# Performance work log

Hardware: AMD Instinct MI355X
Metric: run time of the kernel (lower is better)

Reference implementation:

```python
import jax, jax.numpy as jnp
import numpy as np

T = 5          # temporal frames
WS = 8         # window size (square)
HEADS = 6
DIM = 192      # output channels; qkv input channels = 3*DIM
SHIFT = WS // 2
HDIM = DIM // HEADS
SCALE = HDIM ** -0.5
N = T * WS * WS  # tokens per window = 320


def _rel_index():
    # Faithful replication of the torch buffer construction (including the
    # quirk that the dw channel gets no offset).
    coords = np.stack(np.meshgrid(np.arange(T), np.arange(WS), np.arange(WS), indexing='ij'))
    cf = coords.reshape(3, -1)                      # (3, N)
    rel = (cf[:, :, None] - cf[:, None, :]).transpose(1, 2, 0).astype(np.int64)
    rel[:, :, 0] += WS - 1                          # dt channel
    rel[:, :, 1] += WS - 1                          # dh channel
    rel[:, :, 0] *= 2 * WS - 1
    return rel.sum(-1)                               # (N, N) int

REL_INDEX = jnp.asarray(_rel_index())


def setup_inputs() -> dict:
    key = jax.random.key(0)
    k1, k2, k3, k4 = jax.random.split(key, 4)
    B, H, W = 2, 64, 64
    C = 3 * DIM
    qkv = jax.random.normal(k1, (B, T * H * W, C), jnp.float32)
    bias_table = jax.random.normal(k2, ((T * 2 * WS - 1) * (2 * WS - 1), HEADS), jnp.float32) * 0.02
    proj_w = jax.random.normal(k3, (DIM, DIM), jnp.float32) / np.sqrt(DIM)
    proj_b = jax.random.normal(k4, (DIM,), jnp.float32) * 0.01
    # Standard Swin shifted-window attention mask, tiled over T (t-outer order).
    img = np.zeros((H, W), np.float32)
    cnt = 0
    sls = (slice(0, -WS), slice(-WS, -SHIFT), slice(-SHIFT, None))
    for hs in sls:
        for ws_ in sls:
            img[hs, ws_] = cnt
            cnt += 1
    mw = img.reshape(H // WS, WS, W // WS, WS).transpose(0, 2, 1, 3).reshape(-1, WS * WS)
    mw = np.tile(mw, (1, T))                         # (nW, N)
    am = mw[:, None, :] - mw[:, :, None]
    mask = jnp.asarray(np.where(am != 0, -100.0, 0.0).astype(np.float32))
    return {'qkv': qkv, 'bias_table': bias_table, 'proj_w': proj_w,
            'proj_b': proj_b, 'mask': mask, 'H': H, 'W': W}


def reference(qkv, bias_table, proj_w, proj_b, mask, H, W):
    B, L, C = qkv.shape
    x = qkv.reshape(B, T, H, W, C)
    # cyclic shift
    x = jnp.roll(x, shift=(-SHIFT, -SHIFT), axis=(2, 3))
    # window partition -> (B*nW, N, C)
    x = x.reshape(B, T, H // WS, WS, W // WS, WS, C)
    x = x.transpose(0, 2, 4, 1, 3, 5, 6).reshape(-1, N, C)
    B_ = x.shape[0]
    qkv_ = x.reshape(B_, N, 3, HEADS, HDIM).transpose(2, 0, 3, 1, 4)  # (3,B_,h,N,d)
    q, k, v = qkv_[0] * SCALE, qkv_[1], qkv_[2]
    attn = jnp.einsum('bhqd,bhkd->bhqk', q, k)       # (B_, h, N, N)
    rpb = bias_table[REL_INDEX.reshape(-1)].reshape(N, N, HEADS).transpose(2, 0, 1)
    attn = attn + rpb[None]
    nW = mask.shape[0]
    attn = attn.reshape(B_ // nW, nW, HEADS, N, N) + mask[None, :, None]
    attn = jax.nn.softmax(attn.reshape(B_, HEADS, N, N), axis=-1)
    out = jnp.einsum('bhqk,bhkd->bhqd', attn, v)     # (B_, h, N, d)
    out = out.transpose(0, 2, 1, 3).reshape(B_, N, DIM)
    out = out @ proj_w.T + proj_b
    # window reverse -> (B, T, H, W, DIM)
    out = out.reshape(B, H // WS, W // WS, T, WS, WS, DIM)
    out = out.transpose(0, 3, 1, 4, 2, 5, 6).reshape(B, T, H, W, DIM)
    out = jnp.roll(out, shift=(SHIFT, SHIFT), axis=(2, 3))
    return out.reshape(B, T * H * W, DIM)
```

## Files before the change

kernel.cpp:

```cpp
#include <hip/hip_runtime.h>
#include <hip/hip_bf16.h>

#define TT      5
#define NHEADS  6
#define DIMC    192
#define SHIFT_  4
#define HDIM_   32
#define NTOK    320
#define NWIN    64
#define BATCH   2
#define LOG2E   1.44269504088896f
#define SCALE_LOG2E (0.17677669529663687f * 1.44269504088896f)
#define NEGMASK (-100.0f * 1.44269504088896f)

typedef short short8v __attribute__((ext_vector_type(8)));
typedef float floatx4 __attribute__((ext_vector_type(4)));
union FragU { uint4 u; short8v s; };

static __device__ __forceinline__ float bf16lo(unsigned u) {
    union { unsigned i; float f; } x; x.i = u << 16; return x.f;
}
static __device__ __forceinline__ float bf16hi(unsigned u) {
    union { unsigned i; float f; } x; x.i = u & 0xffff0000u; return x.f;
}
static __device__ __forceinline__ unsigned short bf16b(float f) {
    __hip_bfloat16 h = __float2bfloat16(f);
    unsigned short u; __builtin_memcpy(&u, &h, 2); return u;
}
static __device__ __forceinline__ unsigned pk2(float a, float b) {
    return (unsigned)bf16b(a) | ((unsigned)bf16b(b) << 16);
}
static __device__ __forceinline__ unsigned pk2h(float a, float b) {
    unsigned ua = __float_as_uint(a), ub = __float_as_uint(b);
    return ((ua + 0x8000u) >> 16) | ((ub + 0x8000u) & 0xffff0000u);
}
static __device__ __forceinline__ float fexp2(float x) {
    float r;
    asm("v_exp_f32 %0, %1" : "=v"(r) : "v"(x));
    return r;
}

static __device__ __forceinline__ bool detect_bf16(const unsigned* q) {
    uint4 w = ((const uint4*)q)[threadIdx.x & 63];
    int cnt = 0;
    unsigned e;
    e = (w.x >> 7) & 0xffu; cnt += (e >= 100u && e <= 135u);
    e = (w.y >> 7) & 0xffu; cnt += (e >= 100u && e <= 135u);
    e = (w.z >> 7) & 0xffu; cnt += (e >= 100u && e <= 135u);
    e = (w.w >> 7) & 0xffu; cnt += (e >= 100u && e <= 135u);
    unsigned long long m = __ballot(cnt >= 2);
    return __popcll(m) >= 32;
}

__global__ __launch_bounds__(NTOK) void attn_mfma(
    const void* __restrict__ qkv_raw,
    const float* __restrict__ rpb,
    __hip_bfloat16* __restrict__ win_out)
{
    const bool isbf = detect_bf16((const unsigned*)qkv_raw);
    const int bid = blockIdx.x;
    const int b_  = bid / NHEADS;
    const int h   = bid - b_ * NHEADS;
    const int bb  = b_ >> 6;
    const int wdx = b_ & 63;
    const int wi  = wdx >> 3, wj = wdx & 7;
    const int tid = threadIdx.x;
    const int w    = tid >> 6;
    const int lane = tid & 63;
    const int l15  = lane & 15;
    const int quad = lane >> 4;
    const int g    = lane >> 3;
    const int li   = lane & 7;

    __shared__ unsigned short sVT[32 * 328];

    {
        const int btok = w * 64;
        if (!isbf) {
            const float* q32 = (const float*)qkv_raw;
            #pragma unroll
            for (int r = 0; r < 8; r++) {
                const int token = btok + r * 8 + g;
                const int t = token >> 6, s = token & 63;
                const int gh = (wi * 8 + (s >> 3) + SHIFT_) & 63;
                const int gw = (wj * 8 + (s & 7) + SHIFT_) & 63;
                const long grow = (long)bb * (TT * 64 * 64) + t * 4096 + gh * 64 + gw;
                const float4 vv = *(const float4*)(q32 + grow * (3 * DIMC) + 2 * DIMC + h * HDIM_ + li * 4);
                const int d0 = li * 4;
                sVT[(d0 + 0) * 328 + token] = bf16b(vv.x);
                sVT[(d0 + 1) * 328 + token] = bf16b(vv.y);
                sVT[(d0 + 2) * 328 + token] = bf16b(vv.z);
                sVT[(d0 + 3) * 328 + token] = bf16b(vv.w);
            }
        } else {
            const unsigned short* q16 = (const unsigned short*)qkv_raw;
            #pragma unroll
            for (int r = 0; r < 8; r++) {
                const int token = btok + r * 8 + g;
                const int t = token >> 6, s = token & 63;
                const int gh = (wi * 8 + (s >> 3) + SHIFT_) & 63;
                const int gw = (wj * 8 + (s & 7) + SHIFT_) & 63;
                const long grow = (long)bb * (TT * 64 * 64) + t * 4096 + gh * 64 + gw;
                const uint2 vv = *(const uint2*)(q16 + grow * (3 * DIMC) + 2 * DIMC + h * HDIM_ + li * 4);
                const int d0 = li * 4;
                sVT[(d0 + 0) * 328 + token] = (unsigned short)(vv.x & 0xffffu);
                sVT[(d0 + 1) * 328 + token] = (unsigned short)(vv.x >> 16);
                sVT[(d0 + 2) * 328 + token] = (unsigned short)(vv.y & 0xffffu);
                sVT[(d0 + 3) * 328 + token] = (unsigned short)(vv.y >> 16);
            }
        }
    }

    FragU qf[4];
    int labq[4];
    const float* rq[4];
    #pragma unroll
    for (int jq = 0; jq < 4; jq++) {
        const int qtok = w * 64 + jq * 16 + l15;
        const int t = qtok >> 6, s = qtok & 63, hl = s >> 3, wl = s & 7;
        rq[jq] = rpb + ((h * NTOK + qtok) * NTOK);
        const int hh = wi * 8 + hl, ww = wj * 8 + wl;
        labq[jq] = ((hh < 56) ? 0 : ((hh < 60) ? 1 : 2)) * 3 +
                   ((ww < 56) ? 0 : ((ww < 60) ? 1 : 2));
        const int gh = (wi * 8 + hl + SHIFT_) & 63;
        const int gw = (wj * 8 + wl + SHIFT_) & 63;
        const long grow = (long)bb * (TT * 64 * 64) + t * 4096 + gh * 64 + gw;
        if (!isbf) {
            const float* qp = (const float*)qkv_raw + grow * (3 * DIMC) + h * HDIM_ + quad * 8;
            qf[jq].u = make_uint4(
                pk2(qp[0]*SCALE_LOG2E, qp[1]*SCALE_LOG2E), pk2(qp[2]*SCALE_LOG2E, qp[3]*SCALE_LOG2E),
                pk2(qp[4]*SCALE_LOG2E, qp[5]*SCALE_LOG2E), pk2(qp[6]*SCALE_LOG2E, qp[7]*SCALE_LOG2E));
        } else {
            const uint4 uu = *(const uint4*)((const __hip_bfloat16*)qkv_raw + grow * (3 * DIMC) + h * HDIM_ + quad * 8);
            qf[jq].u = make_uint4(
                pk2(bf16lo(uu.x)*SCALE_LOG2E, bf16hi(uu.x)*SCALE_LOG2E),
                pk2(bf16lo(uu.y)*SCALE_LOG2E, bf16hi(uu.y)*SCALE_LOG2E),
                pk2(bf16lo(uu.z)*SCALE_LOG2E, bf16hi(uu.z)*SCALE_LOG2E),
                pk2(bf16lo(uu.w)*SCALE_LOG2E, bf16hi(uu.w)*SCALE_LOG2E));
        }
    }
    __syncthreads();

    const int koff0 = ((l15 >> 2) << 3) + (l15 & 3);

    const floatx4 z4 = {0.f, 0.f, 0.f, 0.f};
    floatx4 oacc[4][2];
    #pragma unroll
    for (int i = 0; i < 4; i++) { oacc[i][0] = z4; oacc[i][1] = z4; }
    float rs[4] = {0.f, 0.f, 0.f, 0.f};

    for (int kb = 0; kb < 10; kb++) {
        FragU kf0, kf1;
        {
            const int tok0 = kb * 32 + koff0;
            const int t0 = tok0 >> 6, s0 = tok0 & 63;
            const int gh0 = (wi * 8 + (s0 >> 3) + SHIFT_) & 63;
            const int gw0 = (wj * 8 + (s0 & 7) + SHIFT_) & 63;
            const long grow0 = (long)bb * (TT * 64 * 64) + t0 * 4096 + gh0 * 64 + gw0;
            const int tok1 = tok0 + 4;
            const int t1 = tok1 >> 6, s1 = tok1 & 63;
            const int gh1 = (wi * 8 + (s1 >> 3) + SHIFT_) & 63;
            const int gw1 = (wj * 8 + (s1 & 7) + SHIFT_) & 63;
            const long grow1 = (long)bb * (TT * 64 * 64) + t1 * 4096 + gh1 * 64 + gw1;
            if (!isbf) {
                const float* kp0 = (const float*)qkv_raw + grow0 * (3 * DIMC) + DIMC + h * HDIM_ + quad * 8;
                const float* kp1 = (const float*)qkv_raw + grow1 * (3 * DIMC) + DIMC + h * HDIM_ + quad * 8;
                const float4 a0 = *(const float4*)kp0, b0 = *(const float4*)(kp0 + 4);
                const float4 a1 = *(const float4*)kp1, b1 = *(const float4*)(kp1 + 4);
                kf0.u = make_uint4(pk2(a0.x, a0.y), pk2(a0.z, a0.w), pk2(b0.x, b0.y), pk2(b0.z, b0.w));
                kf1.u = make_uint4(pk2(a1.x, a1.y), pk2(a1.z, a1.w), pk2(b1.x, b1.y), pk2(b1.z, b1.w));
            } else {
                kf0.u = *(const uint4*)((const __hip_bfloat16*)qkv_raw + grow0 * (3 * DIMC) + DIMC + h * HDIM_ + quad * 8);
                kf1.u = *(const uint4*)((const __hip_bfloat16*)qkv_raw + grow1 * (3 * DIMC) + DIMC + h * HDIM_ + quad * 8);
            }
        }

        FragU vf0, vf1;
        vf0.u = *(const uint4*)&sVT[l15 * 328 + kb * 32 + quad * 8];
        vf1.u = *(const uint4*)&sVT[(16 + l15) * 328 + kb * 32 + quad * 8];

        float4 rb0[4], rb1[4];
        #pragma unroll
        for (int jq = 0; jq < 4; jq++) {
            const float* rp = rq[jq] + kb * 32 + quad * 8;
            rb0[jq] = *(const float4*)rp;
            rb1[jq] = *(const float4*)(rp + 4);
        }

        floatx4 sv0[4], sv1[4];
        #pragma unroll
        for (int jq = 0; jq < 4; jq++)
            sv0[jq] = __builtin_amdgcn_mfma_f32_16x16x32_bf16(kf0.s, qf[jq].s, z4, 0, 0, 0);
        #pragma unroll
        for (int jq = 0; jq < 4; jq++)
            sv1[jq] = __builtin_amdgcn_mfma_f32_16x16x32_bf16(kf1.s, qf[jq].s, z4, 0, 0, 0);

        const int sh   = (kb & 1) * 4 + quad;
        const int rhk  = (wi == 7) ? ((sh < 4) ? 1 : 2) : 0;
        const int lab0 = rhk * 3 + ((wj == 7) ? 1 : 0);
        const int lab1 = rhk * 3 + ((wj == 7) ? 2 : 0);

        #pragma unroll
        for (int jq = 0; jq < 4; jq++) {
            const float m0 = (lab0 != labq[jq]) ? NEGMASK : 0.f;
            const float m1 = (lab1 != labq[jq]) ? NEGMASK : 0.f;
            float e0[4], e1[4];
            e0[0] = fexp2(sv0[jq][0] + rb0[jq].x + m0);
            e0[1] = fexp2(sv0[jq][1] + rb0[jq].y + m0);
            e0[2] = fexp2(sv0[jq][2] + rb0[jq].z + m0);
            e0[3] = fexp2(sv0[jq][3] + rb0[jq].w + m0);
            e1[0] = fexp2(sv1[jq][0] + rb1[jq].x + m1);
            e1[1] = fexp2(sv1[jq][1] + rb1[jq].y + m1);
            e1[2] = fexp2(sv1[jq][2] + rb1[jq].z + m1);
            e1[3] = fexp2(sv1[jq][3] + rb1[jq].w + m1);
            rs[jq] += ((e0[0] + e0[1]) + (e0[2] + e0[3]))
                    + ((e1[0] + e1[1]) + (e1[2] + e1[3]));
            FragU pf;
            pf.u.x = pk2h(e0[0], e0[1]); pf.u.y = pk2h(e0[2], e0[3]);
            pf.u.z = pk2h(e1[0], e1[1]); pf.u.w = pk2h(e1[2], e1[3]);
            oacc[jq][0] = __builtin_amdgcn_mfma_f32_16x16x32_bf16(vf0.s, pf.s, oacc[jq][0], 0, 0, 0);
            oacc[jq][1] = __builtin_amdgcn_mfma_f32_16x16x32_bf16(vf1.s, pf.s, oacc[jq][1], 0, 0, 0);
        }
    }

    unsigned short* wp = (unsigned short*)win_out;
    #pragma unroll
    for (int jq = 0; jq < 4; jq++) {
        float r = rs[jq];
        r += __shfl_xor(r, 16);
        r += __shfl_xor(r, 32);
        const float inv = 1.0f / r;
        const long ob = ((long)b_ * NTOK + (w * 64 + jq * 16 + l15)) * DIMC + h * HDIM_ + quad * 4;
        #pragma unroll
        for (int nt = 0; nt < 2; nt++) {
            const floatx4 o = oacc[jq][nt];
            *(uint2*)&wp[ob + nt * 16] =
                make_uint2(pk2(o[0] * inv, o[1] * inv), pk2(o[2] * inv, o[3] * inv));
        }
    }
}

__global__ __launch_bounds__(256) void prep_all(
    const void* __restrict__ w_raw, const void* __restrict__ b_raw,
    const void* __restrict__ bias_raw,
    const unsigned* __restrict__ sniff,
    unsigned short* __restrict__ wbf, float* __restrict__ bf32,
    float* __restrict__ rpb)
{
    const bool isbf = detect_bf16(sniff);
    const int g = blockIdx.x * 256 + threadIdx.x;
    if (g < 36864) {
        if (!isbf) wbf[g] = bf16b(((const float*)w_raw)[g]);
        else       wbf[g] = ((const unsigned short*)w_raw)[g];
    }
    if (g < 192) {
        bf32[g] = isbf
            ? __bfloat162float(((const __hip_bfloat16*)b_raw)[g])
            : ((const float*)b_raw)[g];
    }
    const int h = g / (NTOK * NTOK);
    const int r = g - h * (NTOK * NTOK);
    const int q = r / NTOK;
    const int k = r - q * NTOK;
    const int cnq = (q >> 6) * 15 + ((q >> 3) & 7) + (q & 7);
    const int cnk = (k >> 6) * 15 + ((k >> 3) & 7) + (k & 7);
    const int idx = (cnq - cnk + 112) * NHEADS + h;
    const float v = isbf
        ? __bfloat162float(((const __hip_bfloat16*)bias_raw)[idx])
        : ((const float*)bias_raw)[idx];
    rpb[g] = v * LOG2E;
}

__global__ __launch_bounds__(256) void proj_mfma(
    const __hip_bfloat16* __restrict__ win,
    const unsigned short* __restrict__ wbf,
    const float* __restrict__ bf32,
    const unsigned* __restrict__ sniff,
    void* __restrict__ out_raw)
{
    const bool isbf = detect_bf16(sniff);
    const int tid  = threadIdx.x;
    const int w    = tid >> 6;
    const int lane = tid & 63;
    const int l15  = lane & 15;
    const int quad = lane >> 4;
    const int tok0 = blockIdx.x * 64 + w * 16;

    __shared__ unsigned short sX[64 * 200];

    {
        const unsigned short* src = (const unsigned short*)win
                                  + (long)blockIdx.x * 64 * DIMC;
        #pragma unroll
        for (int it = 0; it < 6; it++) {
            const int j   = it * 256 + tid;
            const int tok = j / 24;
            const int d8  = j - tok * 24;
            const uint4 v = *(const uint4*)(src + j * 8);
            *(uint4*)&sX[tok * 200 + d8 * 8] = v;
        }
    }
    __syncthreads();

    const floatx4 z4 = {0.f, 0.f, 0.f, 0.f};
    floatx4 acc[12];
    #pragma unroll
    for (int nt = 0; nt < 12; nt++) acc[nt] = z4;

    #pragma unroll
    for (int ks = 0; ks < 6; ks++) {
        FragU xf;
        xf.u = *(const uint4*)&sX[(w * 16 + l15) * 200 + ks * 32 + quad * 8];
        #pragma unroll
        for (int nt = 0; nt < 12; nt++) {
            FragU wf;
            wf.u = *(const uint4*)(wbf + (nt * 16 + l15) * DIMC + ks * 32 + quad * 8);
            acc[nt] = __builtin_amdgcn_mfma_f32_16x16x32_bf16(wf.s, xf.s, acc[nt], 0, 0, 0);
        }
    }

    const int token = tok0 + l15;
    const int bw = token / NTOK;
    const int nn = token - bw * NTOK;
    const int bb = bw >> 6, wdx = bw & 63, wi2 = wdx >> 3, wj2 = wdx & 7;
    const int t = nn >> 6, s2 = nn & 63, hl = s2 >> 3, wl = s2 & 7;
    const int gh = (wi2 * 8 + hl + SHIFT_) & 63;
    const int gw = (wj2 * 8 + wl + SHIFT_) & 63;
    const long rowoff = ((long)bb * (TT * 64 * 64) + t * 4096 + gh * 64 + gw) * DIMC;

    #pragma unroll
    for (int nt = 0; nt < 12; nt++) {
        const float4 bv = *(const float4*)&bf32[nt * 16 + quad * 4];
        const float o0 = acc[nt][0] + bv.x, o1 = acc[nt][1] + bv.y;
        const float o2 = acc[nt][2] + bv.z, o3 = acc[nt][3] + bv.w;
        const long off = rowoff + nt * 16 + quad * 4;
        if (!isbf) {
            *(float4*)((float*)out_raw + off) = make_float4(o0, o1, o2, o3);
        } else {
            *(uint2*)((unsigned short*)out_raw + off) = make_uint2(pk2(o0, o1), pk2(o2, o3));
        }
    }
}

extern "C" void kernel_launch(void* const* d_in, const int* in_sizes, int n_in,
                              void* d_out, int out_size, void* d_ws, size_t ws_size,
                              hipStream_t stream)
{
    (void)in_sizes; (void)n_in; (void)out_size; (void)ws_size;
    const void* qkv        = d_in[0];
    const void* bias_table = d_in[1];
    const void* proj_w     = d_in[2];
    const void* proj_b     = d_in[3];

    __hip_bfloat16* win = (__hip_bfloat16*)d_ws;
    unsigned short* wbf = (unsigned short*)((char*)d_ws + 15728640);
    float*          bfb = (float*)((char*)d_ws + 15802368);
    float*          rpb = (float*)((char*)d_ws + 15803136);

    prep_all<<<dim3(2400), 256, 0, stream>>>(proj_w, proj_b, bias_table,
                                             (const unsigned*)qkv, wbf, bfb, rpb);
    attn_mfma<<<dim3(BATCH * NWIN * NHEADS), NTOK, 0, stream>>>(qkv, rpb, win);
    proj_mfma<<<dim3(BATCH * NWIN * NTOK / 64), 256, 0, stream>>>(
        win, wbf, bfb, (const unsigned*)qkv, d_out);
}
```

Before: 262.8 us.

## Split attention into one-wave blocks and gather V fragments directly from global

The attention kernel now launches one 64-thread block per (window, head, query-slab) instead of one 320-thread block per (window, head). The shared-memory V transpose and its barrier are removed, so each wave builds its V MFMA fragments with scalar strided global loads. This is meant to raise occupancy and drop the LDS staging and sync. In exchange every wave re-reads all of V for its window-head, five times the V traffic, through uncoalesced 2-byte or 4-byte element loads.

```diff
diff --git a/kernel.cpp b/kernel.cpp
--- a/kernel.cpp
+++ b/kernel.cpp
@@ -15,7 +15,7 @@
 
 typedef short short8v __attribute__((ext_vector_type(8)));
 typedef float floatx4 __attribute__((ext_vector_type(4)));
-union FragU { uint4 u; short8v s; };
+union FragU { uint4 u; short8v s; unsigned short h[8]; };
 
 static __device__ __forceinline__ float bf16lo(unsigned u) {
     union { unsigned i; float f; } x; x.i = u << 16; return x.f;
@@ -52,64 +52,23 @@
     return __popcll(m) >= 32;
 }
 
-__global__ __launch_bounds__(NTOK) void attn_mfma(
+__global__ __launch_bounds__(64) void attn_mfma(
     const void* __restrict__ qkv_raw,
     const float* __restrict__ rpb,
     __hip_bfloat16* __restrict__ win_out)
 {
     const bool isbf = detect_bf16((const unsigned*)qkv_raw);
     const int bid = blockIdx.x;
-    const int b_  = bid / NHEADS;
-    const int h   = bid - b_ * NHEADS;
+    const int w   = bid % 5;
+    const int bh  = bid / 5;
+    const int h   = bh % NHEADS;
+    const int b_  = bh / NHEADS;
     const int bb  = b_ >> 6;
     const int wdx = b_ & 63;
     const int wi  = wdx >> 3, wj = wdx & 7;
-    const int tid = threadIdx.x;
-    const int w    = tid >> 6;
-    const int lane = tid & 63;
+    const int lane = threadIdx.x;
     const int l15  = lane & 15;
     const int quad = lane >> 4;
-    const int g    = lane >> 3;
-    const int li   = lane & 7;
-
-    __shared__ unsigned short sVT[32 * 328];
-
-    {
-        const int btok = w * 64;
-        if (!isbf) {
-            const float* q32 = (const float*)qkv_raw;
-            #pragma unroll
-            for (int r = 0; r < 8; r++) {
-                const int token = btok + r * 8 + g;
-                const int t = token >> 6, s = token & 63;
-                const int gh = (wi * 8 + (s >> 3) + SHIFT_) & 63;
-                const int gw = (wj * 8 + (s & 7) + SHIFT_) & 63;
-                const long grow = (long)bb * (TT * 64 * 64) + t * 4096 + gh * 64 + gw;
-                const float4 vv = *(const float4*)(q32 + grow * (3 * DIMC) + 2 * DIMC + h * HDIM_ + li * 4);
-                const int d0 = li * 4;
-                sVT[(d0 + 0) * 328 + token] = bf16b(vv.x);
-                sVT[(d0 + 1) * 328 + token] = bf16b(vv.y);
-                sVT[(d0 + 2) * 328 + token] = bf16b(vv.z);
-                sVT[(d0 + 3) * 328 + token] = bf16b(vv.w);
-            }
-        } else {
-            const unsigned short* q16 = (const unsigned short*)qkv_raw;
-            #pragma unroll
-            for (int r = 0; r < 8; r++) {
-                const int token = btok + r * 8 + g;
-                const int t = token >> 6, s = token & 63;
-                const int gh = (wi * 8 + (s >> 3) + SHIFT_) & 63;
-                const int gw = (wj * 8 + (s & 7) + SHIFT_) & 63;
-                const long grow = (long)bb * (TT * 64 * 64) + t * 4096 + gh * 64 + gw;
-                const uint2 vv = *(const uint2*)(q16 + grow * (3 * DIMC) + 2 * DIMC + h * HDIM_ + li * 4);
-                const int d0 = li * 4;
-                sVT[(d0 + 0) * 328 + token] = (unsigned short)(vv.x & 0xffffu);
-                sVT[(d0 + 1) * 328 + token] = (unsigned short)(vv.x >> 16);
-                sVT[(d0 + 2) * 328 + token] = (unsigned short)(vv.y & 0xffffu);
-                sVT[(d0 + 3) * 328 + token] = (unsigned short)(vv.y >> 16);
-            }
-        }
-    }
 
     FragU qf[4];
     int labq[4];
@@ -139,7 +98,6 @@
                 pk2(bf16lo(uu.w)*SCALE_LOG2E, bf16hi(uu.w)*SCALE_LOG2E));
         }
     }
-    __syncthreads();
 
     const int koff0 = ((l15 >> 2) << 3) + (l15 & 3);
 
@@ -176,8 +134,31 @@
         }
 
         FragU vf0, vf1;
-        vf0.u = *(const uint4*)&sVT[l15 * 328 + kb * 32 + quad * 8];
-        vf1.u = *(const uint4*)&sVT[(16 + l15) * 328 + kb * 32 + quad * 8];
+        {
+            const int tb = kb * 32 + quad * 8;
+            const int t  = tb >> 6, hl = (tb & 63) >> 3;
+            const int gh = (wi * 8 + hl + SHIFT_) & 63;
+            const long growb = (long)bb * (TT * 64 * 64) + t * 4096 + gh * 64;
+            if (!isbf) {
+                const float* q32 = (const float*)qkv_raw;
+                #pragma unroll
+                for (int j = 0; j < 8; j++) {
+                    const int gw = (wj * 8 + j + SHIFT_) & 63;
+                    const float* vp = q32 + (growb + gw) * (3 * DIMC) + 2 * DIMC + h * HDIM_;
+                    vf0.h[j] = bf16b(vp[l15]);
+                    vf1.h[j] = bf16b(vp[16 + l15]);
+                }
+            } else {
+                const unsigned short* q16 = (const unsigned short*)qkv_raw;
+                #pragma unroll
+                for (int j = 0; j < 8; j++) {
+                    const int gw = (wj * 8 + j + SHIFT_) & 63;
+                    const unsigned short* vp = q16 + (growb + gw) * (3 * DIMC) + 2 * DIMC + h * HDIM_;
+                    vf0.h[j] = vp[l15];
+                    vf1.h[j] = vp[16 + l15];
+                }
+            }
+        }
 
         float4 rb0[4], rb1[4];
         #pragma unroll
@@ -359,7 +340,7 @@
 
     prep_all<<<dim3(2400), 256, 0, stream>>>(proj_w, proj_b, bias_table,
                                              (const unsigned*)qkv, wbf, bfb, rpb);
-    attn_mfma<<<dim3(BATCH * NWIN * NHEADS), NTOK, 0, stream>>>(qkv, rpb, win);
+    attn_mfma<<<dim3(BATCH * NWIN * NHEADS * 5), 64, 0, stream>>>(qkv, rpb, win);
     proj_mfma<<<dim3(BATCH * NWIN * NTOK / 64), 256, 0, stream>>>(
         win, wbf, bfb, (const unsigned*)qkv, d_out);
 }
```

Result: faster. 253.7 us (-3.5%).
